# Optimization experiments

Hardware: AMD Instinct MI355X
Metric: run time of the kernel (lower is better)

Reference implementation:

```python
import jax, jax.numpy as jnp
import numpy as np

H8, W8 = 64, 64
H4, W4 = 128, 128
C_LAT, C_HI = 256, 128
N_Q = 1024
ORIG_H, ORIG_W = 512, 512
NUM_ITERS = 4
TEMP = 20.0
DIM = 4 + C_HI + C_LAT        # 388 mixer output dim
IN_DIM = DIM + 3 * 49         # 535 mixer input dim
HID = 512


def _unit(v):
    return v / jnp.sqrt(jnp.maximum(jnp.sum(v * v, axis=-1, keepdims=True), 1e-12))


def setup_inputs() -> dict:
    key = jax.random.key(0)
    ks = jax.random.split(key, 20)
    fg = _unit(jax.random.normal(ks[0], (1, H8, W8, C_LAT), jnp.float32))
    hg = _unit(jax.random.normal(ks[1], (1, H4, W4, C_HI), jnp.float32))
    qf = _unit(jax.random.normal(ks[2], (1, N_Q, C_LAT), jnp.float32))
    hq = _unit(jax.random.normal(ks[3], (1, N_Q, C_HI), jnp.float32))
    p = lambda k, s, sc=0.05: sc * jax.random.normal(k, s, jnp.float32)
    return dict(
        feature_grid=fg, hires_feats_grid=hg, query_feats=qf, hires_query_feats=hq,
        hid1_w=p(ks[4], (16, 1, 3, 3)), hid1_b=jnp.zeros((16,), jnp.float32),
        hid2_w=p(ks[5], (1, 16, 3, 3)), hid2_b=jnp.zeros((1,), jnp.float32),
        hid3_w=p(ks[6], (32, 16, 3, 3)), hid3_b=jnp.zeros((32,), jnp.float32),
        hid4_w=p(ks[7], (32, 16)), hid4_b=jnp.zeros((16,), jnp.float32),
        occ_w=p(ks[8], (16, 2)), occ_b=jnp.zeros((2,), jnp.float32),
        mix_in_w=p(ks[9], (IN_DIM, HID), 0.02), mix_in_b=jnp.zeros((HID,), jnp.float32),
        mix_out_w=p(ks[10], (HID, DIM), 0.02), mix_out_b=jnp.zeros((DIM,), jnp.float32),
    )


def _conv2d(x, w, b, stride, pad):
    y = jax.lax.conv_general_dilated(x, w, (stride, stride), pad,
                                     dimension_numbers=('NCHW', 'OIHW', 'NCHW'))
    return y + b[None, :, None, None]


def _bilinear_sample(grid, coords):
    # grid [H,W,C]; coords [..., 2] as (y, x); edge-clamped bilinear gather.
    H, W = grid.shape[0], grid.shape[1]
    y, x = coords[..., 0], coords[..., 1]
    y0f, x0f = jnp.floor(y), jnp.floor(x)
    wy, wx = (y - y0f)[..., None], (x - x0f)[..., None]
    y0 = jnp.clip(y0f.astype(jnp.int32), 0, H - 1)
    y1 = jnp.clip(y0f.astype(jnp.int32) + 1, 0, H - 1)
    x0 = jnp.clip(x0f.astype(jnp.int32), 0, W - 1)
    x1 = jnp.clip(x0f.astype(jnp.int32) + 1, 0, W - 1)
    g00, g01 = grid[y0, x0], grid[y0, x1]
    g10, g11 = grid[y1, x0], grid[y1, x1]
    return (g00 * (1 - wy) * (1 - wx) + g01 * (1 - wy) * wx
            + g10 * wy * (1 - wx) + g11 * wy * wx)


def _forward(fg, hg, qf, hq, hid1_w, hid1_b, hid2_w, hid2_b, hid3_w, hid3_b,
             hid4_w, hid4_b, occ_w, occ_b, mix_in_w, mix_in_b, mix_out_w, mix_out_b):
    # --- tracks_from_cost_volume ---
    cv = jnp.einsum('bnc,bhwc->bnhw', qf, fg)                 # [1,N,64,64]
    b, n, h, w = cv.shape
    x = cv.reshape(b * n, 1, h, w)
    occ_map = jax.nn.relu(_conv2d(x, hid1_w, hid1_b, 1, 'SAME'))   # [bn,16,h,w]
    pmap = _conv2d(occ_map, hid2_w, hid2_b, 1, 'SAME').reshape(b * n, h * w)
    heat = jax.nn.softmax(pmap * TEMP, axis=-1).reshape(b * n, h, w)
    ey = jnp.einsum('bhw,h->b', heat, jnp.arange(h, dtype=jnp.float32))
    ex = jnp.einsum('bhw,w->b', heat, jnp.arange(w, dtype=jnp.float32))
    points = jnp.stack([ex * (ORIG_W / w), ey * (ORIG_H / h)], -1).reshape(b, n, 2)
    op = jnp.pad(occ_map, ((0, 0), (0, 0), (0, 2), (0, 2)))
    o3 = jax.nn.relu(_conv2d(op, hid3_w, hid3_b, 2, 'VALID'))
    o3 = o3.mean((-1, -2))                                     # [bn,32]
    o3 = jax.nn.relu(o3 @ hid4_w + hid4_b)
    o3 = (o3 @ occ_w + occ_b).reshape(b, n, 2)
    occ, expd = o3[..., 0], o3[..., 1]

    # --- iterative pips refinement ---
    cy, cx = jnp.meshgrid(jnp.arange(-3, 4), jnp.arange(-3, 4), indexing='ij')
    ctx = jnp.stack([cy, cx], -1).reshape(-1, 2).astype(jnp.float32)   # [49,2] (dy,dx)
    fg_avg = fg.reshape(1, H8 // 2, 2, W8 // 2, 2, C_LAT).mean((2, 4))
    pyramid = [hg, fg, fg_avg]
    feats = jnp.concatenate([hq, qf], -1)                      # [1,N,384]
    pos = points
    for it in range(NUM_ITERS):
        if it == 0:
            queries = [hq[0], qf[0], qf[0]]
        else:
            queries = [feats[0, :, :C_HI], feats[0, :, C_HI:], feats[0, :, C_HI:]]
        corrs = []
        for grid, q in zip(pyramid, queries):
            gh, gw = grid.shape[1], grid.shape[2]
            scale = jnp.array([gw / ORIG_W, gh / ORIG_H], jnp.float32)
            c = (pos[0] * scale)[:, ::-1]                      # (x,y)->(y,x), [N,2]
            coords2 = c[:, None, :] + ctx[None]                # [N,49,2]
            nb = _bilinear_sample(grid[0], coords2)            # [N,49,C]
            corrs.append(jnp.einsum('nsc,nc->ns', nb, q))
        corrs = jnp.concatenate(corrs, -1)[None]               # [1,N,147]
        mlp_in = jnp.concatenate([jnp.zeros_like(pos), occ[..., None],
                                  expd[..., None], feats, corrs], -1)
        res = jax.nn.gelu(mlp_in @ mix_in_w + mix_in_b) @ mix_out_w + mix_out_b
        pos = pos + res[..., :2]
        occ = occ + res[..., 2]
        expd = expd + res[..., 3]
        feats = feats + res[..., 4:]
    return jnp.concatenate([pos, occ[..., None], expd[..., None]], -1)  # [1,N,4]


def reference(feature_grid, hires_feats_grid, query_feats, hires_query_feats,
              hid1_w, hid1_b, hid2_w, hid2_b, hid3_w, hid3_b, hid4_w, hid4_b,
              occ_w, occ_b, mix_in_w, mix_in_b, mix_out_w, mix_out_b):
    return _forward(feature_grid, hires_feats_grid, query_feats, hires_query_feats,
                    hid1_w, hid1_b, hid2_w, hid2_b, hid3_w, hid3_b, hid4_w, hid4_b,
                    occ_w, occ_b, mix_in_w, mix_in_b, mix_out_w, mix_out_b)
```

## Files before the change

### kernel.cpp

```cpp
#include <hip/hip_runtime.h>
#include <hip/hip_bf16.h>
#include <math.h>


#define NQ 1024
#define TEMPF 20.0f
#define DIMV 388
#define INDIM 535
#define KPAD 544
#define HID 512

#define WS_CV      0
#define WS_FGAVG   (WS_CV + NQ*4096)
#define WS_POS     (WS_FGAVG + 262144)
#define WS_OCC     (WS_POS + NQ*2)
#define WS_EXPD    (WS_OCC + NQ)
#define WS_FEATS   (WS_EXPD + NQ)
#define WS_MLPIN   (WS_FEATS + NQ*384)
#define WS_HIDDEN  (WS_MLPIN + NQ*KPAD)
#define WS_W3B     (WS_HIDDEN + NQ*HID)
#define WS_PART    (WS_MLPIN + 278528)
#define WS_SUM3    WS_HIDDEN
#define WS_WIT     WS_CV
#define WS_WOT     (WS_CV + 139264)

#define OP 72
#define CVP 68

typedef __attribute__((ext_vector_type(8))) short bf16x8;
typedef __attribute__((ext_vector_type(4))) float f32x4;

__global__ __launch_bounds__(256) void k_prep(
    const float* __restrict__ fg, const float* __restrict__ qf,
    const float* __restrict__ hq, const float* __restrict__ w3,
    float* __restrict__ ws) {
  int i = blockIdx.x * 256 + threadIdx.x;
  if (i < 262144) {
    int c = i & 255, ox = (i >> 8) & 31, oy = i >> 13;
    const float* b = fg + (((oy * 2) * 64 + ox * 2) << 8) + c;
    ws[WS_FGAVG + i] = 0.25f * (b[0] + b[256] + b[16384] + b[16384 + 256]);
  } else if (i < 262144 + 393216) {
    int j = i - 262144;
    int n = j / 384, c = j - n * 384;
    ws[WS_FEATS + j] = (c < 128) ? hq[n * 128 + c] : qf[n * 256 + c - 128];
  } else if (i < 262144 + 393216 + 5120) {
    int j = i - (262144 + 393216);
    int e = j & 7, qd = (j >> 3) & 3, nl = (j >> 5) & 15;
    int nt = (j >> 9) & 1, kt = j >> 10;
    int k = kt * 32 + qd * 8 + e;
    int ic = k & 15, tap = k >> 4;
    int oc = nt * 16 + nl;
    float v = (tap < 9) ? w3[(oc * 16 + ic) * 9 + tap] : 0.f;
    ((__hip_bfloat16*)(ws + WS_W3B))[j] = __float2bfloat16(v);
  } else if (i < 262144 + 393216 + 5120 + 524288) {
    int j = i - (262144 + 393216 + 5120);
    ws[WS_SUM3 + j] = 0.f;
  }
}

__global__ __launch_bounds__(256) void k_cv(
    const float* __restrict__ qf, const float* __restrict__ fg,
    float* __restrict__ ws) {
  __shared__ __hip_bfloat16 A_s[32 * 32];
  __shared__ __hip_bfloat16 B_s[64 * 32];
  const int t = threadIdx.x;
  const int wv = t >> 6, lane = t & 63;
  const int wm = wv & 1, wn = wv >> 1;
  const int quad = lane >> 4, nl = lane & 15;
  const int p0 = blockIdx.x * 64, m0 = blockIdx.y * 32;
  f32x4 acc0 = {0.f, 0.f, 0.f, 0.f};
  f32x4 acc1 = {0.f, 0.f, 0.f, 0.f};

  for (int k0 = 0; k0 < 256; k0 += 32) {
    {
      int r = t >> 3, c = t & 7;
      float4 v = *(const float4*)&qf[(m0 + r) * 256 + k0 + c * 4];
      union { __hip_bfloat16 h[4]; uint2 u; } pk;
      pk.h[0] = __float2bfloat16(v.x); pk.h[1] = __float2bfloat16(v.y);
      pk.h[2] = __float2bfloat16(v.z); pk.h[3] = __float2bfloat16(v.w);
      *(uint2*)&A_s[r * 32 + c * 4] = pk.u;
    }
    {
      int r = t >> 2, c = t & 3;
      const float* src = &fg[(p0 + r) * 256 + k0 + c * 8];
      float4 v0 = *(const float4*)src;
      float4 v1 = *(const float4*)(src + 4);
      union { __hip_bfloat16 h[8]; uint4 u; } pk;
      pk.h[0] = __float2bfloat16(v0.x); pk.h[1] = __float2bfloat16(v0.y);
      pk.h[2] = __float2bfloat16(v0.z); pk.h[3] = __float2bfloat16(v0.w);
      pk.h[4] = __float2bfloat16(v1.x); pk.h[5] = __float2bfloat16(v1.y);
      pk.h[6] = __float2bfloat16(v1.z); pk.h[7] = __float2bfloat16(v1.w);
      *(uint4*)&B_s[r * 32 + c * 8] = pk.u;
    }
    __syncthreads();
    bf16x8 a = *(const bf16x8*)&A_s[(16 * wm + nl) * 32 + quad * 8];
    bf16x8 b0 = *(const bf16x8*)&B_s[(32 * wn + nl) * 32 + quad * 8];
    bf16x8 b1 = *(const bf16x8*)&B_s[(32 * wn + 16 + nl) * 32 + quad * 8];
    acc0 = __builtin_amdgcn_mfma_f32_16x16x32_bf16(a, b0, acc0, 0, 0, 0);
    acc1 = __builtin_amdgcn_mfma_f32_16x16x32_bf16(a, b1, acc1, 0, 0, 0);
    __syncthreads();
  }
#pragma unroll
  for (int nt = 0; nt < 2; nt++) {
    int n = p0 + 32 * wn + nt * 16 + nl;
#pragma unroll
    for (int r = 0; r < 4; r++) {
      int m = m0 + 16 * wm + quad * 4 + r;
      ws[WS_CV + m * 4096 + n] = (nt ? acc1[r] : acc0[r]);
    }
  }
}

__global__ __launch_bounds__(256, 4) void k_head_stripe(
    const float* __restrict__ h1w, const float* __restrict__ h1b,
    const float* __restrict__ h2w, const float* __restrict__ h2b,
    const float* __restrict__ h3b, float* __restrict__ ws) {
  __shared__ float cvs[8 * CVP];
  __shared__ float occ[6 * 16 * OP];

  const int bx = blockIdx.x;
  const int q = bx >> 4, st = bx & 15;
  const int y0 = st * 4;
  const int t = threadIdx.x;
  const int wv = t >> 6, lane = t & 63;
  const int role = (wv + bx) & 3;
  const float* cv = ws + WS_CV + q * 4096;

  if (t < 192) {
    int rc = t >> 1, side = t & 1;
    *(float4*)&occ[rc * OP + side * 68] = make_float4(0.f, 0.f, 0.f, 0.f);
  }
  if (st == 0 || st == 15) {
    int r = (st == 0) ? 0 : 5;
    for (int i = t; i < 16 * 18; i += 256)
      *(float4*)&occ[(r * 16 + (i / 18)) * OP + (i % 18) * 4] =
          make_float4(0.f, 0.f, 0.f, 0.f);
  }
#pragma unroll
  for (int j = 0; j < 2; j++) {
    int i = t + 256 * j;
    int lr = i >> 6, x = i & 63;
    int g = y0 - 2 + lr;
    cvs[lr * CVP + x + 1] = (g >= 0 && g < 64) ? cv[g * 64 + x] : 0.f;
  }
  if (t < 32) {
    int rr = t >> 2, c = t & 3;
    cvs[rr * CVP + ((c == 0) ? 0 : (64 + c))] = 0.f;
  }
  __syncthreads();

  {
    const int chg = wv * 4;
    const int xg = lane & 15, rsel = lane >> 4;
    const int x0 = xg * 4;
    float w1r[4][9], b1r[4];
#pragma unroll
    for (int k = 0; k < 4; k++) {
      b1r[k] = h1b[chg + k];
#pragma unroll
      for (int j = 0; j < 9; j++) w1r[k][j] = h1w[(chg + k) * 9 + j];
    }
#pragma unroll
    for (int p = 0; p < 2; p++) {
      int r = p * 4 + rsel;
      int yo = y0 - 1 + r;
      if (r < 6 && yo >= 0 && yo <= 63) {
        float rb[3][6];
#pragma unroll
        for (int ky = 0; ky < 3; ky++) {
          const float* cp = &cvs[(r + ky) * CVP + x0];
          float4 a4 = *(const float4*)cp;
          float2 b2 = *(const float2*)(cp + 4);
          rb[ky][0] = a4.x; rb[ky][1] = a4.y; rb[ky][2] = a4.z;
          rb[ky][3] = a4.w; rb[ky][4] = b2.x; rb[ky][5] = b2.y;
        }
#pragma unroll
        for (int k = 0; k < 4; k++) {
          float o[4];
#pragma unroll
          for (int px = 0; px < 4; px++) {
            float a = b1r[k];
#pragma unroll
            for (int ky = 0; ky < 3; ky++)
              a += w1r[k][3 * ky] * rb[ky][px] +
                   w1r[k][3 * ky + 1] * rb[ky][px + 1] +
                   w1r[k][3 * ky + 2] * rb[ky][px + 2];
            o[px] = fmaxf(a, 0.f);
          }
          *(float4*)&occ[(r * 16 + chg + k) * OP + x0 + 4] =
              make_float4(o[0], o[1], o[2], o[3]);
        }
      }
    }
  }
  __syncthreads();

  if (role == 1 || role == 2) {
    const __hip_bfloat16* W3B = (const __hip_bfloat16*)(ws + WS_W3B);
    const int oyl = role - 1;
    const int nl = lane & 15;
    const int qd = lane >> 4, qh = qd >> 1, ql = qd & 1;
    f32x4 acc00 = {0.f,0.f,0.f,0.f}, acc01 = {0.f,0.f,0.f,0.f};
    f32x4 acc10 = {0.f,0.f,0.f,0.f}, acc11 = {0.f,0.f,0.f,0.f};
#pragma unroll
    for (int kt = 0; kt < 5; kt++) {
      int tap = kt * 2 + qh;
      int tv = (tap < 9) ? tap : 0;
      int ky = (tv >= 6) ? 2 : ((tv >= 3) ? 1 : 0);
      int kx = tv - 3 * ky;
      const float* ap =
          &occ[((2 * oyl + 1 + ky) * 16 + ql * 8) * OP + 4 + kx + 2 * nl];
      union { bf16x8 v; __hip_bfloat16 h[8]; } a0u, a1u;
      if (tap < 9) {
#pragma unroll
        for (int j = 0; j < 8; j++) {
          a0u.h[j] = __float2bfloat16(ap[j * OP]);
          a1u.h[j] = __float2bfloat16(ap[j * OP + 32]);
        }
      } else {
#pragma unroll
        for (int j = 0; j < 8; j++) {
          a0u.h[j] = __float2bfloat16(0.f);
          a1u.h[j] = __float2bfloat16(0.f);
        }
      }
      bf16x8 b0 = *(const bf16x8*)&W3B[((kt * 2 + 0) * 16 + nl) * 32 + qd * 8];
      bf16x8 b1 = *(const bf16x8*)&W3B[((kt * 2 + 1) * 16 + nl) * 32 + qd * 8];
      acc00 = __builtin_amdgcn_mfma_f32_16x16x32_bf16(a0u.v, b0, acc00, 0, 0, 0);
      acc01 = __builtin_amdgcn_mfma_f32_16x16x32_bf16(a0u.v, b1, acc01, 0, 0, 0);
      acc10 = __builtin_amdgcn_mfma_f32_16x16x32_bf16(a1u.v, b0, acc10, 0, 0, 0);
      acc11 = __builtin_amdgcn_mfma_f32_16x16x32_bf16(a1u.v, b1, acc11, 0, 0, 0);
    }
    float bb0 = h3b[nl], bb1 = h3b[16 + nl];
    float s0 = 0.f, s1 = 0.f;
#pragma unroll
    for (int r = 0; r < 4; r++) {
      s0 += fmaxf(acc00[r] + bb0, 0.f) + fmaxf(acc10[r] + bb0, 0.f);
      s1 += fmaxf(acc01[r] + bb1, 0.f) + fmaxf(acc11[r] + bb1, 0.f);
    }
    s0 += __shfl_xor(s0, 16); s0 += __shfl_xor(s0, 32);
    s1 += __shfl_xor(s1, 16); s1 += __shfl_xor(s1, 32);
    if (lane < 16) {
      atomicAdd(&ws[WS_SUM3 + (q * 16 + st) * 32 + nl], s0);
      atomicAdd(&ws[WS_SUM3 + (q * 16 + st) * 32 + 16 + nl], s1);
    }
  } else {
    const int rl = ((role == 3) ? 2 : 0) + (lane >> 5);
    const int yg = y0 + rl;
    const int x0 = (lane & 31) * 2;
    float pa = 0.f, pb = 0.f;
    for (int ch = 0; ch < 16; ch++) {
#pragma unroll
      for (int ky = 0; ky < 3; ky++) {
        const float* bp = &occ[((rl + ky) * 16 + ch) * OP + x0];
        float f0 = bp[3];
        float2 fm = *(const float2*)(bp + 4);
        float f3 = bp[6];
        float wa = h2w[ch * 9 + 3 * ky], wb = h2w[ch * 9 + 3 * ky + 1],
              wc = h2w[ch * 9 + 3 * ky + 2];
        pa += wa * f0 + wb * fm.x + wc * fm.y;
        pb += wa * fm.x + wb * fm.y + wc * f3;
      }
    }
    float bb = h2b[0];
    float v0 = (pa + bb) * TEMPF, v1 = (pb + bb) * TEMPF;
    float mg = fmaxf(v0, v1);
#pragma unroll
    for (int off = 1; off < 64; off <<= 1) mg = fmaxf(mg, __shfl_xor(mg, off));
    float e0 = __expf(v0 - mg), e1 = __expf(v1 - mg);
    float s = e0 + e1;
    float sx = e0 * (float)x0 + e1 * (float)(x0 + 1);
    float sy = s * (float)yg;
#pragma unroll
    for (int off = 1; off < 64; off <<= 1) {
      s += __shfl_xor(s, off);
      sx += __shfl_xor(sx, off);
      sy += __shfl_xor(sy, off);
    }
    if (lane == 0) {
      int slot = q * 32 + st * 2 + ((role == 3) ? 1 : 0);
      *(float4*)&ws[WS_PART + slot * 4] = make_float4(mg, s, sx, sy);
    }
  }
}

__global__ __launch_bounds__(256) void k_merge_cvt(
    const float* __restrict__ w4, const float* __restrict__ b4,
    const float* __restrict__ w5, const float* __restrict__ b5,
    const float* __restrict__ wi, const float* __restrict__ wo,
    float* __restrict__ ws) {
  {
    int i = blockIdx.x * 256 + threadIdx.x;
    __hip_bfloat16* WIT = (__hip_bfloat16*)(ws + WS_WIT);
    __hip_bfloat16* WOT = (__hip_bfloat16*)(ws + WS_WOT);
    if (i < 278528) {
      int n = i / KPAD, k = i - n * KPAD;
      float v = (k < INDIM) ? wi[k * HID + n] : 0.f;
      WIT[i] = __float2bfloat16(v);
    } else if (i < 278528 + 229376) {
      int j = i - 278528;
      int n = j >> 9, k = j & 511;
      float v = (n < DIMV) ? wo[k * DIMV + n] : 0.f;
      WOT[j] = __float2bfloat16(v);
    }
  }
  if (blockIdx.x >= 256) return;

  __shared__ float sums_s[4][32];
  __shared__ float o4s[4][16];
  int t = threadIdx.x, wv = t >> 6, lane = t & 63;
  int q = blockIdx.x * 4 + wv;

  float M = -1e30f, S = 0.f, SX = 0.f, SY = 0.f;
  if (lane < 32) {
    float4 pv = *(const float4*)&ws[WS_PART + (q * 32 + lane) * 4];
    M = pv.x; S = pv.y; SX = pv.z; SY = pv.w;
  }
#pragma unroll
  for (int off = 1; off < 64; off <<= 1) {
    float Mo = __shfl_xor(M, off), So = __shfl_xor(S, off);
    float SXo = __shfl_xor(SX, off), SYo = __shfl_xor(SY, off);
    float Mn = fmaxf(M, Mo);
    float c1 = __expf(M - Mn), c2 = __expf(Mo - Mn);
    S = S * c1 + So * c2; SX = SX * c1 + SXo * c2; SY = SY * c1 + SYo * c2;
    M = Mn;
  }
  if (lane == 0) {
    ws[WS_POS + q * 2 + 0] = (SX / S) * 8.0f;
    ws[WS_POS + q * 2 + 1] = (SY / S) * 8.0f;
  }

  int ch = lane & 31, half = lane >> 5;
  float sm = 0.f;
#pragma unroll
  for (int s8 = 0; s8 < 8; s8++)
    sm += ws[WS_SUM3 + (q * 16 + half * 8 + s8) * 32 + ch];
  sm += __shfl_xor(sm, 32);
  if (lane < 32) sums_s[wv][lane] = sm * (1.f / 1024.f);
  __syncthreads();
  if (lane < 16) {
    float a = b4[lane];
#pragma unroll
    for (int i = 0; i < 32; i++) a += sums_s[wv][i] * w4[i * 16 + lane];
    o4s[wv][lane] = fmaxf(a, 0.f);
  }
  __syncthreads();
  if (lane < 2) {
    float r = b5[lane];
#pragma unroll
    for (int j = 0; j < 16; j++) r += o4s[wv][j] * w5[j * 2 + lane];
    if (lane == 0) ws[WS_OCC + q] = r;
    else           ws[WS_EXPD + q] = r;
  }
}

__global__ __launch_bounds__(256) void k_corr(
    const float* __restrict__ fg, const float* __restrict__ hg,
    float* __restrict__ ws) {
  __shared__ float qs[384];
  __shared__ float dbuf[3][64];
  int t = threadIdx.x;
  int wv = t >> 6, lane = t & 63;
  int cl = lane & 15, sub = lane >> 4;
  int n = blockIdx.x;
  const float* feats = ws + WS_FEATS + n * 384;
  float posx = ws[WS_POS + n * 2 + 0];
  float posy = ws[WS_POS + n * 2 + 1];
  __hip_bfloat16* mi = (__hip_bfloat16*)(ws + WS_MLPIN) + n * KPAD;

  for (int col = t; col < 384; col += 256) {
    float v = feats[col];
    qs[col] = v;
    mi[4 + col] = __float2bfloat16(v);
  }
  if (t < 4) {
    float v = (t == 2) ? ws[WS_OCC + n] : ((t == 3) ? ws[WS_EXPD + n] : 0.f);
    mi[t] = __float2bfloat16(v);
  }
  __syncthreads();

  float4 qh0 = *(const float4*)&qs[cl * 4];
  float4 qh1 = *(const float4*)&qs[64 + cl * 4];
  float4 qq0 = *(const float4*)&qs[128 + cl * 4];
  float4 qq1 = *(const float4*)&qs[192 + cl * 4];
  float4 qq2 = *(const float4*)&qs[256 + cl * 4];
  float4 qq3 = *(const float4*)&qs[320 + cl * 4];

#pragma unroll
  for (int L = 0; L < 3; L++) {
    const float* grid;
    int Hg, Wg;
    float scl;
    if (L == 0)      { grid = hg;             Hg = 128; Wg = 128; scl = 0.25f; }
    else if (L == 1) { grid = fg;             Hg = 64;  Wg = 64;  scl = 0.125f; }
    else             { grid = ws + WS_FGAVG;  Hg = 32;  Wg = 32;  scl = 0.0625f; }
    float cy = posy * scl, cx = posx * scl;
    int iy = (int)floorf(cy), ix = (int)floorf(cx);
#pragma unroll
    for (int g = 0; g < 4; g++) {
      int p = wv * 16 + g * 4 + sub;
      int a = p >> 3, b = p & 7;
      int row = iy + a - 3; row = row < 0 ? 0 : (row > Hg - 1 ? Hg - 1 : row);
      int col = ix + b - 3; col = col < 0 ? 0 : (col > Wg - 1 ? Wg - 1 : col);
      float acc;
      if (L == 0) {
        const float* gp = grid + (row * Wg + col) * 128 + cl * 4;
        float4 g0 = *(const float4*)gp;
        float4 g1 = *(const float4*)(gp + 64);
        acc = g0.x * qh0.x + g0.y * qh0.y + g0.z * qh0.z + g0.w * qh0.w +
              g1.x * qh1.x + g1.y * qh1.y + g1.z * qh1.z + g1.w * qh1.w;
      } else {
        const float* gp = grid + (row * Wg + col) * 256 + cl * 4;
        float4 g0 = *(const float4*)gp;
        float4 g1 = *(const float4*)(gp + 64);
        float4 g2 = *(const float4*)(gp + 128);
        float4 g3 = *(const float4*)(gp + 192);
        acc = g0.x * qq0.x + g0.y * qq0.y + g0.z * qq0.z + g0.w * qq0.w +
              g1.x * qq1.x + g1.y * qq1.y + g1.z * qq1.z + g1.w * qq1.w +
              g2.x * qq2.x + g2.y * qq2.y + g2.z * qq2.z + g2.w * qq2.w +
              g3.x * qq3.x + g3.y * qq3.y + g3.z * qq3.z + g3.w * qq3.w;
      }
      acc += __shfl_xor(acc, 1);
      acc += __shfl_xor(acc, 2);
      acc += __shfl_xor(acc, 4);
      acc += __shfl_xor(acc, 8);
      if (cl == 0) dbuf[L][p] = acc;
    }
  }
  __syncthreads();

  if (t < 147) {
    int L = t / 49, s = t - L * 49;
    int sa = s / 7, sb = s - sa * 7;
    float scl = (L == 0) ? 0.25f : ((L == 1) ? 0.125f : 0.0625f);
    float cy = posy * scl, cx = posx * scl;
    float wy = cy - floorf(cy), wx = cx - floorf(cx);
    int i00 = sa * 8 + sb;
    float d00 = dbuf[L][i00], d01 = dbuf[L][i00 + 1];
    float d10 = dbuf[L][i00 + 8], d11 = dbuf[L][i00 + 9];
    float corr = (1.f - wy) * (1.f - wx) * d00 + (1.f - wy) * wx * d01 +
                 wy * (1.f - wx) * d10 + wy * wx * d11;
    mi[388 + t] = __float2bfloat16(corr);
  }
}

__device__ __forceinline__ float gelu_tanh(float x) {
  float z = 0.7978845608028654f * (x + 0.044715f * x * x * x);
  z = fminf(fmaxf(z, -15.f), 15.f);
  float e = __expf(2.f * z);
  float th = (e - 1.f) / (e + 1.f);
  return 0.5f * x * (1.f + th);
}

__global__ __launch_bounds__(256) void k_mix1(
    const float* __restrict__ bias, float* __restrict__ ws) {
  __shared__ __hip_bfloat16 A_s[32 * 32];
  __shared__ __hip_bfloat16 B_s[64 * 32];
  const int t = threadIdx.x;
  const int wv = t >> 6, lane = t & 63;
  const int wm = wv & 1, wn = wv >> 1;
  const int quad = lane >> 4, nl = lane & 15;
  const int n0 = blockIdx.x * 64, m0 = blockIdx.y * 32;
  const unsigned short* Abf = (const unsigned short*)(ws + WS_MLPIN);
  const unsigned short* WIT = (const unsigned short*)(ws + WS_WIT);
  f32x4 acc0 = {0.f, 0.f, 0.f, 0.f};
  f32x4 acc1 = {0.f, 0.f, 0.f, 0.f};

  for (int k0 = 0; k0 < KPAD; k0 += 32) {
    if (t < 128) {
      int r = t >> 2, c = t & 3;
      *(uint4*)&A_s[r * 32 + c * 8] =
          *(const uint4*)&Abf[(m0 + r) * KPAD + k0 + c * 8];
    }
    {
      int r = t >> 2, c = t & 3;
      *(uint4*)&B_s[r * 32 + c * 8] =
          *(const uint4*)&WIT[(n0 + r) * KPAD + k0 + c * 8];
    }
    __syncthreads();
    bf16x8 a = *(const bf16x8*)&A_s[(16 * wm + nl) * 32 + quad * 8];
    bf16x8 b0 = *(const bf16x8*)&B_s[(32 * wn + nl) * 32 + quad * 8];
    bf16x8 b1 = *(const bf16x8*)&B_s[(32 * wn + 16 + nl) * 32 + quad * 8];
    acc0 = __builtin_amdgcn_mfma_f32_16x16x32_bf16(a, b0, acc0, 0, 0, 0);
    acc1 = __builtin_amdgcn_mfma_f32_16x16x32_bf16(a, b1, acc1, 0, 0, 0);
    __syncthreads();
  }

  __hip_bfloat16* Hd = (__hip_bfloat16*)(ws + WS_HIDDEN);
#pragma unroll
  for (int nt = 0; nt < 2; nt++) {
    int nn = n0 + 32 * wn + nt * 16 + nl;
    float bv = bias[nn];
#pragma unroll
    for (int r = 0; r < 4; r++) {
      int m = m0 + 16 * wm + quad * 4 + r;
      float v = gelu_tanh((nt ? acc1[r] : acc0[r]) + bv);
      Hd[m * HID + nn] = __float2bfloat16(v);
    }
  }
}

__global__ __launch_bounds__(256) void k_mix2(
    const float* __restrict__ bias, float* __restrict__ ws,
    float* __restrict__ out) {
  __shared__ __hip_bfloat16 A_s[32 * 32];
  __shared__ __hip_bfloat16 B_s[64 * 32];
  const int t = threadIdx.x;
  const int wv = t >> 6, lane = t & 63;
  const int wm = wv & 1, wn = wv >> 1;
  const int quad = lane >> 4, nl = lane & 15;
  const int n0 = blockIdx.x * 64, m0 = blockIdx.y * 32;
  const unsigned short* Abf = (const unsigned short*)(ws + WS_HIDDEN);
  const unsigned short* WOT = (const unsigned short*)(ws + WS_WOT);
  f32x4 acc0 = {0.f, 0.f, 0.f, 0.f};
  f32x4 acc1 = {0.f, 0.f, 0.f, 0.f};

  for (int k0 = 0; k0 < HID; k0 += 32) {
    if (t < 128) {
      int r = t >> 2, c = t & 3;
      *(uint4*)&A_s[r * 32 + c * 8] =
          *(const uint4*)&Abf[(m0 + r) * HID + k0 + c * 8];
    }
    {
      int r = t >> 2, c = t & 3;
      *(uint4*)&B_s[r * 32 + c * 8] =
          *(const uint4*)&WOT[(n0 + r) * HID + k0 + c * 8];
    }
    __syncthreads();
    bf16x8 a = *(const bf16x8*)&A_s[(16 * wm + nl) * 32 + quad * 8];
    bf16x8 b0 = *(const bf16x8*)&B_s[(32 * wn + nl) * 32 + quad * 8];
    bf16x8 b1 = *(const bf16x8*)&B_s[(32 * wn + 16 + nl) * 32 + quad * 8];
    acc0 = __builtin_amdgcn_mfma_f32_16x16x32_bf16(a, b0, acc0, 0, 0, 0);
    acc1 = __builtin_amdgcn_mfma_f32_16x16x32_bf16(a, b1, acc1, 0, 0, 0);
    __syncthreads();
  }

#pragma unroll
  for (int nt = 0; nt < 2; nt++) {
    int col = n0 + 32 * wn + nt * 16 + nl;
    if (col >= DIMV) continue;
    float bv = bias[col];
#pragma unroll
    for (int r = 0; r < 4; r++) {
      int m = m0 + 16 * wm + quad * 4 + r;
      float rr = (nt ? acc1[r] : acc0[r]) + bv;
      if (col < 2) {
        float v = ws[WS_POS + m * 2 + col] + rr;
        ws[WS_POS + m * 2 + col] = v;
        out[m * 4 + col] = v;
      } else if (col == 2) {
        float v = ws[WS_OCC + m] + rr;
        ws[WS_OCC + m] = v;
        out[m * 4 + 2] = v;
      } else if (col == 3) {
        float v = ws[WS_EXPD + m] + rr;
        ws[WS_EXPD + m] = v;
        out[m * 4 + 3] = v;
      } else {
        ws[WS_FEATS + m * 384 + (col - 4)] += rr;
      }
    }
  }
}

extern "C" void kernel_launch(void* const* d_in, const int* in_sizes, int n_in,
                              void* d_out, int out_size, void* d_ws, size_t ws_size,
                              hipStream_t stream) {
  const float* fg = (const float*)d_in[0];
  const float* hg = (const float*)d_in[1];
  const float* qf = (const float*)d_in[2];
  const float* hq = (const float*)d_in[3];
  const float* w1 = (const float*)d_in[4];
  const float* b1 = (const float*)d_in[5];
  const float* w2 = (const float*)d_in[6];
  const float* b2 = (const float*)d_in[7];
  const float* w3 = (const float*)d_in[8];
  const float* b3 = (const float*)d_in[9];
  const float* w4 = (const float*)d_in[10];
  const float* b4 = (const float*)d_in[11];
  const float* w5 = (const float*)d_in[12];
  const float* b5 = (const float*)d_in[13];
  const float* wi = (const float*)d_in[14];
  const float* bi = (const float*)d_in[15];
  const float* wo = (const float*)d_in[16];
  const float* bo = (const float*)d_in[17];
  float* ws = (float*)d_ws;
  float* out = (float*)d_out;

  k_prep<<<4628, 256, 0, stream>>>(fg, qf, hq, w3, ws);
  k_cv<<<dim3(64, 32), 256, 0, stream>>>(qf, fg, ws);
  k_head_stripe<<<16384, 256, 0, stream>>>(w1, b1, w2, b2, b3, ws);
  k_merge_cvt<<<1984, 256, 0, stream>>>(w4, b4, w5, b5, wi, wo, ws);
  for (int it = 0; it < 4; it++) {
    k_corr<<<1024, 256, 0, stream>>>(fg, hg, ws);
    k_mix1<<<dim3(8, 32), 256, 0, stream>>>(bi, ws);
    k_mix2<<<dim3(7, 32), 256, 0, stream>>>(bo, ws, out);
  }
}
```

Before: 340.8 us.

## Fuse mixer MLP GEMMs into one kernel with hidden layer kept in LDS

Merges the two mixer GEMM kernels into a single kernel where each block handles 16 query rows. It computes the GELU hidden layer into shared memory, then the output projection, with register double-buffered weight loads and no global hidden buffer. This removes one launch per iteration and the hidden-activation round trip through global memory, but uses only 64 blocks, leaving many CUs idle. It also changes the head conv1 stripe to one pixel per lane, looping over rows instead of using vectorised 4-pixel reads.

```diff
diff --git a/kernel.cpp b/kernel.cpp
--- a/kernel.cpp
+++ b/kernel.cpp
@@ -26,9 +26,12 @@
 
 #define OP 72
 #define CVP 68
+#define HPITCH 520
 
 typedef __attribute__((ext_vector_type(8))) short bf16x8;
 typedef __attribute__((ext_vector_type(4))) float f32x4;
+
+union U4B8 { uint4 u; bf16x8 v; };
 
 __global__ __launch_bounds__(256) void k_prep(
     const float* __restrict__ fg, const float* __restrict__ qf,
@@ -150,9 +153,8 @@
   __syncthreads();
 
   {
+    const int x = lane;
     const int chg = wv * 4;
-    const int xg = lane & 15, rsel = lane >> 4;
-    const int x0 = xg * 4;
     float w1r[4][9], b1r[4];
 #pragma unroll
     for (int k = 0; k < 4; k++) {
@@ -160,35 +162,21 @@
 #pragma unroll
       for (int j = 0; j < 9; j++) w1r[k][j] = h1w[(chg + k) * 9 + j];
     }
-#pragma unroll
-    for (int p = 0; p < 2; p++) {
-      int r = p * 4 + rsel;
+    for (int r = 0; r < 6; r++) {
       int yo = y0 - 1 + r;
-      if (r < 6 && yo >= 0 && yo <= 63) {
-        float rb[3][6];
+      if (yo >= 0 && yo <= 63) {
+        float p[9];
 #pragma unroll
         for (int ky = 0; ky < 3; ky++) {
-          const float* cp = &cvs[(r + ky) * CVP + x0];
-          float4 a4 = *(const float4*)cp;
-          float2 b2 = *(const float2*)(cp + 4);
-          rb[ky][0] = a4.x; rb[ky][1] = a4.y; rb[ky][2] = a4.z;
-          rb[ky][3] = a4.w; rb[ky][4] = b2.x; rb[ky][5] = b2.y;
+          const float* cp = &cvs[(r + ky) * CVP + x];
+          p[3 * ky] = cp[0]; p[3 * ky + 1] = cp[1]; p[3 * ky + 2] = cp[2];
         }
 #pragma unroll
         for (int k = 0; k < 4; k++) {
-          float o[4];
-#pragma unroll
-          for (int px = 0; px < 4; px++) {
-            float a = b1r[k];
-#pragma unroll
-            for (int ky = 0; ky < 3; ky++)
-              a += w1r[k][3 * ky] * rb[ky][px] +
-                   w1r[k][3 * ky + 1] * rb[ky][px + 1] +
-                   w1r[k][3 * ky + 2] * rb[ky][px + 2];
-            o[px] = fmaxf(a, 0.f);
-          }
-          *(float4*)&occ[(r * 16 + chg + k) * OP + x0 + 4] =
-              make_float4(o[0], o[1], o[2], o[3]);
+          float a = b1r[k];
+#pragma unroll
+          for (int j = 0; j < 9; j++) a += w1r[k][j] * p[j];
+          occ[(r * 16 + chg + k) * OP + x + 4] = fmaxf(a, 0.f);
         }
       }
     }
@@ -452,112 +440,102 @@
   return 0.5f * x * (1.f + th);
 }
 
-__global__ __launch_bounds__(256) void k_mix1(
-    const float* __restrict__ bias, float* __restrict__ ws) {
-  __shared__ __hip_bfloat16 A_s[32 * 32];
-  __shared__ __hip_bfloat16 B_s[64 * 32];
+__global__ __launch_bounds__(256) void k_mix(
+    const float* __restrict__ bi, const float* __restrict__ bo,
+    float* __restrict__ ws, float* __restrict__ out) {
+  __shared__ __hip_bfloat16 Hs[16 * HPITCH];
   const int t = threadIdx.x;
   const int wv = t >> 6, lane = t & 63;
-  const int wm = wv & 1, wn = wv >> 1;
   const int quad = lane >> 4, nl = lane & 15;
-  const int n0 = blockIdx.x * 64, m0 = blockIdx.y * 32;
-  const unsigned short* Abf = (const unsigned short*)(ws + WS_MLPIN);
+  const int m0 = blockIdx.x * 16;
+  const unsigned short* MI = (const unsigned short*)(ws + WS_MLPIN);
   const unsigned short* WIT = (const unsigned short*)(ws + WS_WIT);
-  f32x4 acc0 = {0.f, 0.f, 0.f, 0.f};
-  f32x4 acc1 = {0.f, 0.f, 0.f, 0.f};
-
-  for (int k0 = 0; k0 < KPAD; k0 += 32) {
-    if (t < 128) {
-      int r = t >> 2, c = t & 3;
-      *(uint4*)&A_s[r * 32 + c * 8] =
-          *(const uint4*)&Abf[(m0 + r) * KPAD + k0 + c * 8];
-    }
-    {
-      int r = t >> 2, c = t & 3;
-      *(uint4*)&B_s[r * 32 + c * 8] =
-          *(const uint4*)&WIT[(n0 + r) * KPAD + k0 + c * 8];
-    }
-    __syncthreads();
-    bf16x8 a = *(const bf16x8*)&A_s[(16 * wm + nl) * 32 + quad * 8];
-    bf16x8 b0 = *(const bf16x8*)&B_s[(32 * wn + nl) * 32 + quad * 8];
-    bf16x8 b1 = *(const bf16x8*)&B_s[(32 * wn + 16 + nl) * 32 + quad * 8];
-    acc0 = __builtin_amdgcn_mfma_f32_16x16x32_bf16(a, b0, acc0, 0, 0, 0);
-    acc1 = __builtin_amdgcn_mfma_f32_16x16x32_bf16(a, b1, acc1, 0, 0, 0);
-    __syncthreads();
-  }
-
-  __hip_bfloat16* Hd = (__hip_bfloat16*)(ws + WS_HIDDEN);
-#pragma unroll
-  for (int nt = 0; nt < 2; nt++) {
-    int nn = n0 + 32 * wn + nt * 16 + nl;
-    float bv = bias[nn];
-#pragma unroll
-    for (int r = 0; r < 4; r++) {
-      int m = m0 + 16 * wm + quad * 4 + r;
-      float v = gelu_tanh((nt ? acc1[r] : acc0[r]) + bv);
-      Hd[m * HID + nn] = __float2bfloat16(v);
-    }
-  }
-}
-
-__global__ __launch_bounds__(256) void k_mix2(
-    const float* __restrict__ bias, float* __restrict__ ws,
-    float* __restrict__ out) {
-  __shared__ __hip_bfloat16 A_s[32 * 32];
-  __shared__ __hip_bfloat16 B_s[64 * 32];
-  const int t = threadIdx.x;
-  const int wv = t >> 6, lane = t & 63;
-  const int wm = wv & 1, wn = wv >> 1;
-  const int quad = lane >> 4, nl = lane & 15;
-  const int n0 = blockIdx.x * 64, m0 = blockIdx.y * 32;
-  const unsigned short* Abf = (const unsigned short*)(ws + WS_HIDDEN);
   const unsigned short* WOT = (const unsigned short*)(ws + WS_WOT);
-  f32x4 acc0 = {0.f, 0.f, 0.f, 0.f};
-  f32x4 acc1 = {0.f, 0.f, 0.f, 0.f};
-
-  for (int k0 = 0; k0 < HID; k0 += 32) {
-    if (t < 128) {
-      int r = t >> 2, c = t & 3;
-      *(uint4*)&A_s[r * 32 + c * 8] =
-          *(const uint4*)&Abf[(m0 + r) * HID + k0 + c * 8];
-    }
-    {
-      int r = t >> 2, c = t & 3;
-      *(uint4*)&B_s[r * 32 + c * 8] =
-          *(const uint4*)&WOT[(n0 + r) * HID + k0 + c * 8];
-    }
-    __syncthreads();
-    bf16x8 a = *(const bf16x8*)&A_s[(16 * wm + nl) * 32 + quad * 8];
-    bf16x8 b0 = *(const bf16x8*)&B_s[(32 * wn + nl) * 32 + quad * 8];
-    bf16x8 b1 = *(const bf16x8*)&B_s[(32 * wn + 16 + nl) * 32 + quad * 8];
-    acc0 = __builtin_amdgcn_mfma_f32_16x16x32_bf16(a, b0, acc0, 0, 0, 0);
-    acc1 = __builtin_amdgcn_mfma_f32_16x16x32_bf16(a, b1, acc1, 0, 0, 0);
-    __syncthreads();
-  }
-
-#pragma unroll
-  for (int nt = 0; nt < 2; nt++) {
-    int col = n0 + 32 * wn + nt * 16 + nl;
-    if (col >= DIMV) continue;
-    float bv = bias[col];
-#pragma unroll
-    for (int r = 0; r < 4; r++) {
-      int m = m0 + 16 * wm + quad * 4 + r;
-      float rr = (nt ? acc1[r] : acc0[r]) + bv;
-      if (col < 2) {
-        float v = ws[WS_POS + m * 2 + col] + rr;
-        ws[WS_POS + m * 2 + col] = v;
-        out[m * 4 + col] = v;
-      } else if (col == 2) {
-        float v = ws[WS_OCC + m] + rr;
-        ws[WS_OCC + m] = v;
-        out[m * 4 + 2] = v;
-      } else if (col == 3) {
-        float v = ws[WS_EXPD + m] + rr;
-        ws[WS_EXPD + m] = v;
-        out[m * 4 + 3] = v;
-      } else {
-        ws[WS_FEATS + m * 384 + (col - 4)] += rr;
+
+  {
+    f32x4 acc[8];
+#pragma unroll
+    for (int i = 0; i < 8; i++) acc[i] = (f32x4){0.f, 0.f, 0.f, 0.f};
+    const unsigned short* Ap = &MI[(m0 + nl) * KPAD + quad * 8];
+    const unsigned short* Bp = &WIT[(wv * 128 + nl) * KPAD + quad * 8];
+    U4B8 a_c, b_c[8], a_n, b_n[8];
+    a_c.u = *(const uint4*)Ap;
+#pragma unroll
+    for (int i = 0; i < 8; i++) b_c[i].u = *(const uint4*)(Bp + i * 16 * KPAD);
+    for (int k0 = 0; k0 < KPAD; k0 += 32) {
+      if (k0 + 32 < KPAD) {
+        a_n.u = *(const uint4*)(Ap + k0 + 32);
+#pragma unroll
+        for (int i = 0; i < 8; i++)
+          b_n[i].u = *(const uint4*)(Bp + i * 16 * KPAD + k0 + 32);
+      }
+#pragma unroll
+      for (int i = 0; i < 8; i++)
+        acc[i] = __builtin_amdgcn_mfma_f32_16x16x32_bf16(a_c.v, b_c[i].v,
+                                                         acc[i], 0, 0, 0);
+      a_c = a_n;
+#pragma unroll
+      for (int i = 0; i < 8; i++) b_c[i] = b_n[i];
+    }
+#pragma unroll
+    for (int i = 0; i < 8; i++) {
+      int col = wv * 128 + i * 16 + nl;
+      float bv = bi[col];
+#pragma unroll
+      for (int r = 0; r < 4; r++) {
+        int row = quad * 4 + r;
+        Hs[row * HPITCH + col] = __float2bfloat16(gelu_tanh(acc[i][r] + bv));
+      }
+    }
+  }
+  __syncthreads();
+
+  {
+    f32x4 acc[7];
+#pragma unroll
+    for (int i = 0; i < 7; i++) acc[i] = (f32x4){0.f, 0.f, 0.f, 0.f};
+    const unsigned short* Bp = &WOT[(wv * 112 + nl) * HID + quad * 8];
+    U4B8 b_c[7], b_n[7];
+#pragma unroll
+    for (int i = 0; i < 7; i++) b_c[i].u = *(const uint4*)(Bp + i * 16 * HID);
+    for (int k0 = 0; k0 < HID; k0 += 32) {
+      if (k0 + 32 < HID) {
+#pragma unroll
+        for (int i = 0; i < 7; i++)
+          b_n[i].u = *(const uint4*)(Bp + i * 16 * HID + k0 + 32);
+      }
+      bf16x8 a = *(const bf16x8*)&Hs[nl * HPITCH + k0 + quad * 8];
+#pragma unroll
+      for (int i = 0; i < 7; i++)
+        acc[i] = __builtin_amdgcn_mfma_f32_16x16x32_bf16(a, b_c[i].v,
+                                                         acc[i], 0, 0, 0);
+#pragma unroll
+      for (int i = 0; i < 7; i++) b_c[i] = b_n[i];
+    }
+#pragma unroll
+    for (int i = 0; i < 7; i++) {
+      int col = wv * 112 + i * 16 + nl;
+      if (col >= DIMV) continue;
+      float bv = bo[col];
+#pragma unroll
+      for (int r = 0; r < 4; r++) {
+        int m = m0 + quad * 4 + r;
+        float rr = acc[i][r] + bv;
+        if (col < 2) {
+          float v = ws[WS_POS + m * 2 + col] + rr;
+          ws[WS_POS + m * 2 + col] = v;
+          out[m * 4 + col] = v;
+        } else if (col == 2) {
+          float v = ws[WS_OCC + m] + rr;
+          ws[WS_OCC + m] = v;
+          out[m * 4 + 2] = v;
+        } else if (col == 3) {
+          float v = ws[WS_EXPD + m] + rr;
+          ws[WS_EXPD + m] = v;
+          out[m * 4 + 3] = v;
+        } else {
+          ws[WS_FEATS + m * 384 + (col - 4)] += rr;
+        }
       }
     }
   }
@@ -593,7 +571,6 @@
   k_merge_cvt<<<1984, 256, 0, stream>>>(w4, b4, w5, b5, wi, wo, ws);
   for (int it = 0; it < 4; it++) {
     k_corr<<<1024, 256, 0, stream>>>(fg, hg, ws);
-    k_mix1<<<dim3(8, 32), 256, 0, stream>>>(bi, ws);
-    k_mix2<<<dim3(7, 32), 256, 0, stream>>>(bo, ws, out);
-  }
-}
+    k_mix<<<64, 256, 0, stream>>>(bi, bo, ws, out);
+  }
+}
```

Measured after the change: 366.4 us. 7.5% more time.
